# Kernel optimization log

Measured on AMD Instinct MI355X. Metric: run time of the kernel, lower is better.

## Reference

```python
import jax, jax.numpy as jnp
import numpy as np

GRID_RES = 64
BOUND = 1.2

def _coords():
    lin = jnp.linspace(-BOUND, BOUND, GRID_RES, dtype=jnp.float32)
    gx, gy, gz = jnp.meshgrid(lin, lin, lin, indexing='ij')
    return jnp.stack([gx, gy, gz], axis=-1).reshape(-1, 3)  # (R^3, 3)

def setup_inputs() -> dict:
    key = jax.random.key(0)
    ks = jax.random.split(key, 9)
    B, D, H = 2, 512, 512
    s_in = 1.0 / np.sqrt(D + 3)
    s_h = 1.0 / np.sqrt(H)
    return {
        'cad_latent': jax.random.normal(ks[0], (B, D), jnp.float32),
        'W0': jax.random.normal(ks[1], (D + 3, H), jnp.float32) * s_in,
        'b0': jax.random.normal(ks[2], (H,), jnp.float32) * s_in,
        'W1': jax.random.normal(ks[3], (H, H), jnp.float32) * s_h,
        'b1': jax.random.normal(ks[4], (H,), jnp.float32) * s_h,
        'W2': jax.random.normal(ks[5], (H, H), jnp.float32) * s_h,
        'b2': jax.random.normal(ks[6], (H,), jnp.float32) * s_h,
        'W3': jax.random.normal(ks[7], (H, 1), jnp.float32) * s_h,
        'b3': jax.random.normal(ks[8], (1,), jnp.float32) * s_h,
    }

def reference(cad_latent, W0, b0, W1, b1, W2, b2, W3, b3):
    B, D = cad_latent.shape
    coords = _coords()  # (P, 3), P = R^3
    # First layer: concat([latent, coords]) @ W0 decomposed to avoid
    # materializing the broadcast-concatenated (B, P, D+3) tensor.
    lat_part = cad_latent @ W0[:D]          # (B, H)
    coord_part = coords @ W0[D:]            # (P, H)
    h = jax.nn.silu(lat_part[:, None, :] + coord_part[None, :, :] + b0)  # (B, P, H)
    h = jax.nn.silu(h @ W1 + b1)
    h = jax.nn.silu(h @ W2 + b2)
    sdf = h @ W3 + b3                       # (B, P, 1)
    return sdf.reshape(B, GRID_RES, GRID_RES, GRID_RES)
```

## Files before the change

### kernel.cpp

```cpp
#include <hip/hip_runtime.h>

#define H 512
#define MTILE 64
#define NBLK 8192
#define HPAD 520
#define STEPC (2.4f / 63.0f)

typedef _Float16 half8 __attribute__((ext_vector_type(8)));
typedef _Float16 half4_t __attribute__((ext_vector_type(4)));
typedef _Float16 half2_t __attribute__((ext_vector_type(2)));
typedef float floatx4 __attribute__((ext_vector_type(4)));

__device__ inline float silu_f(float x) {
    return __fdividef(x, 1.0f + __expf(-x));
}

__global__ void prep_latw(const float* __restrict__ lat, const float* __restrict__ W0,
                          const float* __restrict__ b0, float* __restrict__ latw) {
    __shared__ float sl[H];
    const int b = blockIdx.x;
    const int j = threadIdx.x;
    sl[j] = lat[b * H + j];
    __syncthreads();
    float acc = b0[j];
#pragma unroll 8
    for (int d = 0; d < H; ++d) acc += sl[d] * W0[d * H + j];
    latw[b * H + j] = acc;
}

__global__ void prep_w16(const float* __restrict__ W1, const float* __restrict__ W2,
                         _Float16* __restrict__ ws) {
    const int id = blockIdx.x * 512 + threadIdx.x;
    const int l = id >> 18;
    const int rem = id & 0x3FFFF;
    const int k = rem >> 9, n = rem & 511;
    const float w = (l == 0 ? W1 : W2)[rem];
    const int kc = k >> 5, q = (k >> 3) & 3, k0 = k & 7;
    ws[((size_t)((l * 16 + kc) * 4 + q) * 512 + n) * 8 + k0] = (_Float16)w;
}

__global__ __launch_bounds__(512, 4) void mesh_main(
    const float* __restrict__ W0, const float* __restrict__ b1,
    const float* __restrict__ b2, const float* __restrict__ W3,
    const float* __restrict__ b3, const float* __restrict__ latw,
    const _Float16* __restrict__ wsB, float* __restrict__ out) {

    __shared__ _Float16 hbuf[MTILE][HPAD];
    __shared__ float partials[8][MTILE];

    const int tid = threadIdx.x;
    const int wave = tid >> 6, lane = tid & 63;
    const int q = lane >> 4, t = lane & 15;
    const int bi = blockIdx.x;
    const int b = bi >> 12;
    const int p0 = (bi & 4095) << 6;
    const float c0 = -1.2f + (float)(p0 >> 12) * STEPC;
    const float c1 = -1.2f + (float)((p0 >> 6) & 63) * STEPC;

    {
        const int cp = tid & 255, mh = tid >> 8;
        const int j0 = cp * 2;
        const float w2c0 = W0[(H + 2) * H + j0];
        const float w2c1 = W0[(H + 2) * H + j0 + 1];
        const float lw0 = latw[b * H + j0]
                        + c0 * W0[(H + 0) * H + j0]
                        + c1 * W0[(H + 1) * H + j0];
        const float lw1 = latw[b * H + j0 + 1]
                        + c0 * W0[(H + 0) * H + j0 + 1]
                        + c1 * W0[(H + 1) * H + j0 + 1];
#pragma unroll 4
        for (int mm = 0; mm < 32; ++mm) {
            const int m = mh * 32 + mm;
            const float c2v = -1.2f + (float)m * STEPC;
            half2_t hv;
            hv[0] = (_Float16)silu_f(lw0 + c2v * w2c0);
            hv[1] = (_Float16)silu_f(lw1 + c2v * w2c1);
            *(half2_t*)&hbuf[m][j0] = hv;
        }
    }

    const _Float16* wsl = wsB + ((size_t)q * 512 + wave * 16 + t) * 8;

    floatx4 acc[4][4];

    auto zero_acc = [&]() {
#pragma unroll
        for (int mf = 0; mf < 4; ++mf)
#pragma unroll
            for (int nt = 0; nt < 4; ++nt) {
                acc[mf][nt][0] = 0.f; acc[mf][nt][1] = 0.f;
                acc[mf][nt][2] = 0.f; acc[mf][nt][3] = 0.f;
            }
    };

    auto loadB = [&](int l, int kc, half8 (&bf)[4]) {
        const _Float16* p = wsl + (size_t)(l * 16 + kc) * 16384;
#pragma unroll
        for (int nt = 0; nt < 4; ++nt)
            bf[nt] = *(const half8*)(p + nt * 1024);
    };

    auto compute = [&](int kc, half8 (&bf)[4]) {
        half8 a[4];
#pragma unroll
        for (int mf = 0; mf < 4; ++mf)
            a[mf] = *(const half8*)&hbuf[mf * 16 + t][kc * 32 + q * 8];
#pragma unroll
        for (int nt = 0; nt < 4; ++nt)
#pragma unroll
            for (int mf = 0; mf < 4; ++mf)
                acc[mf][nt] = __builtin_amdgcn_mfma_f32_16x16x32_f16(bf[nt], a[mf], acc[mf][nt], 0, 0, 0);
    };

    auto run_gemm = [&](int l) {
        half8 B0[4], B1[4];
        loadB(l, 0, B0);
#pragma unroll 1
        for (int kc = 0; kc < 16; kc += 2) {
            loadB(l, kc + 1, B1);
            compute(kc, B0);
            loadB(l, (kc + 2) & 15, B0);
            compute(kc + 1, B1);
        }
    };

    zero_acc();
    __syncthreads();
    run_gemm(0);
    __syncthreads();
    {
        floatx4 b1v[4];
#pragma unroll
        for (int nt = 0; nt < 4; ++nt)
            b1v[nt] = *(const floatx4*)&b1[nt * 128 + wave * 16 + q * 4];
#pragma unroll
        for (int mf = 0; mf < 4; ++mf)
#pragma unroll
            for (int nt = 0; nt < 4; ++nt) {
                half4_t hv;
#pragma unroll
                for (int r = 0; r < 4; ++r)
                    hv[r] = (_Float16)silu_f(acc[mf][nt][r] + b1v[nt][r]);
                *(half4_t*)&hbuf[mf * 16 + t][nt * 128 + wave * 16 + q * 4] = hv;
            }
    }

    zero_acc();
    __syncthreads();
    run_gemm(1);

    {
        floatx4 b2v[4], w3v[4];
#pragma unroll
        for (int nt = 0; nt < 4; ++nt) {
            b2v[nt] = *(const floatx4*)&b2[nt * 128 + wave * 16 + q * 4];
            w3v[nt] = *(const floatx4*)&W3[nt * 128 + wave * 16 + q * 4];
        }
#pragma unroll
        for (int mf = 0; mf < 4; ++mf) {
            float sum = 0.f;
#pragma unroll
            for (int nt = 0; nt < 4; ++nt)
#pragma unroll
                for (int r = 0; r < 4; ++r)
                    sum += silu_f(acc[mf][nt][r] + b2v[nt][r]) * w3v[nt][r];
            sum += __shfl_xor(sum, 16);
            sum += __shfl_xor(sum, 32);
            if (lane < 16) partials[wave][mf * 16 + t] = sum;
        }
    }
    __syncthreads();
    if (tid < MTILE) {
        float o = b3[0];
#pragma unroll
        for (int w = 0; w < 8; ++w) o += partials[w][tid];
        out[(size_t)bi * MTILE + tid] = o;
    }
}

extern "C" void kernel_launch(void* const* d_in, const int* in_sizes, int n_in,
                              void* d_out, int out_size, void* d_ws, size_t ws_size,
                              hipStream_t stream) {
    const float* lat = (const float*)d_in[0];
    const float* W0  = (const float*)d_in[1];
    const float* b0  = (const float*)d_in[2];
    const float* W1  = (const float*)d_in[3];
    const float* b1  = (const float*)d_in[4];
    const float* W2  = (const float*)d_in[5];
    const float* b2  = (const float*)d_in[6];
    const float* W3  = (const float*)d_in[7];
    const float* b3  = (const float*)d_in[8];
    float* out = (float*)d_out;

    float* latw = (float*)d_ws;
    _Float16* wsB = (_Float16*)((char*)d_ws + 4096);

    prep_latw<<<2, 512, 0, stream>>>(lat, W0, b0, latw);
    prep_w16<<<1024, 512, 0, stream>>>(W1, W2, wsB);
    mesh_main<<<NBLK, 512, 0, stream>>>(W0, b1, b2, W3, b3, latw, wsB, out);
}
```

Measured before the change: 817.7 us.

## Reorganize activation LDS buffer into MFMA-fragment-contiguous layout

Replaces the padded row-major activation tile in shared memory with a layout where each lane's 8-element A-fragment sits contiguously in 16-byte groups, so A reads become simple strided 128-bit loads. It also precomputes the per-column first-layer constants once per block into a small LDS buffer, then writes the first layer as full half8 vector stores. The goal is to remove LDS bank conflicts and cut redundant global loads and address arithmetic. In exchange it adds an extra barrier and a more intricate index mapping for the layer-1 writeback.

```diff
diff --git a/kernel.cpp b/kernel.cpp
--- a/kernel.cpp
+++ b/kernel.cpp
@@ -3,13 +3,12 @@
 #define H 512
 #define MTILE 64
 #define NBLK 8192
-#define HPAD 520
 #define STEPC (2.4f / 63.0f)
 
 typedef _Float16 half8 __attribute__((ext_vector_type(8)));
 typedef _Float16 half4_t __attribute__((ext_vector_type(4)));
-typedef _Float16 half2_t __attribute__((ext_vector_type(2)));
 typedef float floatx4 __attribute__((ext_vector_type(4)));
+typedef float floatx2 __attribute__((ext_vector_type(2)));
 
 __device__ inline float silu_f(float x) {
     return __fdividef(x, 1.0f + __expf(-x));
@@ -45,7 +44,8 @@
     const float* __restrict__ b3, const float* __restrict__ latw,
     const _Float16* __restrict__ wsB, float* __restrict__ out) {
 
-    __shared__ _Float16 hbuf[MTILE][HPAD];
+    __shared__ _Float16 hbuf2[4096 * 8];
+    __shared__ float lwbuf[2 * H];
     __shared__ float partials[8][MTILE];
 
     const int tid = threadIdx.x;
@@ -58,28 +58,36 @@
     const float c1 = -1.2f + (float)((p0 >> 6) & 63) * STEPC;
 
     {
-        const int cp = tid & 255, mh = tid >> 8;
-        const int j0 = cp * 2;
-        const float w2c0 = W0[(H + 2) * H + j0];
-        const float w2c1 = W0[(H + 2) * H + j0 + 1];
-        const float lw0 = latw[b * H + j0]
-                        + c0 * W0[(H + 0) * H + j0]
-                        + c1 * W0[(H + 1) * H + j0];
-        const float lw1 = latw[b * H + j0 + 1]
-                        + c0 * W0[(H + 0) * H + j0 + 1]
-                        + c1 * W0[(H + 1) * H + j0 + 1];
-#pragma unroll 4
-        for (int mm = 0; mm < 32; ++mm) {
-            const int m = mh * 32 + mm;
-            const float c2v = -1.2f + (float)m * STEPC;
-            half2_t hv;
-            hv[0] = (_Float16)silu_f(lw0 + c2v * w2c0);
-            hv[1] = (_Float16)silu_f(lw1 + c2v * w2c1);
-            *(half2_t*)&hbuf[m][j0] = hv;
+        const int j = tid;
+        const float lwv = latw[b * H + j]
+                        + c0 * W0[(H + 0) * H + j]
+                        + c1 * W0[(H + 1) * H + j];
+        floatx2 v;
+        v[0] = lwv;
+        v[1] = W0[(H + 2) * H + j];
+        *(floatx2*)&lwbuf[2 * j] = v;
+    }
+    __syncthreads();
+
+    {
+        const float c2v = -1.2f + (float)lane * STEPC;
+#pragma unroll
+        for (int s = 0; s < 8; ++s) {
+            const int g = wave * 8 + s;
+            const floatx4* lp = (const floatx4*)&lwbuf[g * 16];
+            half8 hv;
+#pragma unroll
+            for (int i = 0; i < 4; ++i) {
+                const floatx4 pv = lp[i];
+                hv[2 * i + 0] = (_Float16)silu_f(pv[0] + c2v * pv[1]);
+                hv[2 * i + 1] = (_Float16)silu_f(pv[2] + c2v * pv[3]);
+            }
+            *(half8*)&hbuf2[(g * 64 + lane) * 8] = hv;
         }
     }
 
     const _Float16* wsl = wsB + ((size_t)q * 512 + wave * 16 + t) * 8;
+    const _Float16* hb = hbuf2 + q * 512 + t * 8;
 
     floatx4 acc[4][4];
 
@@ -102,9 +110,10 @@
 
     auto compute = [&](int kc, half8 (&bf)[4]) {
         half8 a[4];
+        const _Float16* hp = hb + kc * 2048;
 #pragma unroll
         for (int mf = 0; mf < 4; ++mf)
-            a[mf] = *(const half8*)&hbuf[mf * 16 + t][kc * 32 + q * 8];
+            a[mf] = *(const half8*)(hp + mf * 128);
 #pragma unroll
         for (int nt = 0; nt < 4; ++nt)
 #pragma unroll
@@ -129,6 +138,8 @@
     run_gemm(0);
     __syncthreads();
     {
+        const int R0 = (wave >> 1) * 4 + (wave & 1) * 2 + (q >> 1);
+        _Float16* wb = hbuf2 + R0 * 512 + t * 8 + (q & 1) * 4;
         floatx4 b1v[4];
 #pragma unroll
         for (int nt = 0; nt < 4; ++nt)
@@ -141,7 +152,7 @@
 #pragma unroll
                 for (int r = 0; r < 4; ++r)
                     hv[r] = (_Float16)silu_f(acc[mf][nt][r] + b1v[nt][r]);
-                *(half4_t*)&hbuf[mf * 16 + t][nt * 128 + wave * 16 + q * 4] = hv;
+                *(half4_t*)(wb + nt * 8192 + mf * 128) = hv;
             }
     }
 
```

After: 811.7 us. No clear change (-0.7%).
